# Optimization experiments

Measured on AMD Instinct MI355X. Metric: run time of the kernel, lower is better.

Reference implementation:

```python
import jax, jax.numpy as jnp
import numpy as np

N_NODES = 50000
N_EDGES = 800000
D_IN = 64
D_OUT = 64


def setup_inputs() -> dict:
    key = jax.random.key(0)
    k1, k2, k3, k4, k5 = jax.random.split(key, 5)
    x = jax.random.normal(k1, (N_NODES, D_IN), dtype=jnp.float32)
    senders = jax.random.randint(k2, (N_EDGES,), 0, N_NODES, dtype=jnp.int32)
    receivers = jax.random.randint(k3, (N_EDGES,), 0, N_NODES, dtype=jnp.int32)
    # eqx.nn.Linear params: weight [out, in], bias [out]
    weight = jax.random.normal(k4, (D_OUT, D_IN), dtype=jnp.float32) / np.sqrt(D_IN)
    bias = jax.random.normal(k5, (D_OUT,), dtype=jnp.float32) * 0.01
    return {"x": x, "senders": senders, "receivers": receivers, "weight": weight, "bias": bias}


def reference(x, senders, receivers, weight, bias):
    n = x.shape[0]
    # jraph.GraphConvolution applies update_node_fn (the Linear) FIRST
    h = x @ weight.T + bias  # [N, D_OUT]
    # add self edges
    self_idx = jnp.arange(n, dtype=senders.dtype)
    cs = jnp.concatenate([senders, self_idx])
    cr = jnp.concatenate([receivers, self_idx])
    ones = jnp.ones(cs.shape, dtype=h.dtype)
    sender_deg = jax.ops.segment_sum(ones, cs, num_segments=n)
    receiver_deg = jax.ops.segment_sum(ones, cr, num_segments=n)
    # symmetric normalization: D^{-1/2} A D^{-1/2}
    h = h * jax.lax.rsqrt(jnp.maximum(sender_deg, 1.0))[:, None]
    h = jax.ops.segment_sum(h[cs], cr, num_segments=n)  # gather -> scatter-add
    h = h * jax.lax.rsqrt(jnp.maximum(receiver_deg, 1.0))[:, None]
    return jax.nn.leaky_relu(h)  # default negative_slope=0.01
```

## Files before the change

kernel.cpp:

```cpp
#include <hip/hip_runtime.h>

#define N_NODES 50000
#define N_EDGES 800000
#define D 64
#define NB 196
#define BSZ 256
#define NSLICE 196
#define E4 (N_EDGES / 4)
#define CAP 64

__device__ __forceinline__ ushort f2bf(float f) {
    unsigned u = __float_as_uint(f);
    unsigned r = u + 0x7fffu + ((u >> 16) & 1u);
    return (ushort)(r >> 16);
}
__device__ __forceinline__ void acc8(const uint4 a, float* acc) {
    acc[0] += __uint_as_float(a.x << 16);
    acc[1] += __uint_as_float(a.x & 0xffff0000u);
    acc[2] += __uint_as_float(a.y << 16);
    acc[3] += __uint_as_float(a.y & 0xffff0000u);
    acc[4] += __uint_as_float(a.z << 16);
    acc[5] += __uint_as_float(a.z & 0xffff0000u);
    acc[6] += __uint_as_float(a.w << 16);
    acc[7] += __uint_as_float(a.w & 0xffff0000u);
}

__global__ __launch_bounds__(1024) void part1_kernel(
        const int* __restrict__ s, const int* __restrict__ r,
        unsigned* __restrict__ prc, unsigned char* __restrict__ psc,
        int* __restrict__ rcnt, int* __restrict__ scnt) {
    __shared__ int rcur[NB], scur[NB];
    const int tid = threadIdx.x, sl = blockIdx.x;
    for (int i = tid; i < NB; i += 1024) { rcur[i] = 0; scur[i] = 0; }
    __syncthreads();

    const size_t cellbase = (size_t)sl * NB * CAP;
    int e4 = sl * 1024 + tid;
    if (e4 < E4) {
        int4 rv = ((const int4*)r)[e4];
        int4 sv = ((const int4*)s)[e4];
        int ri[4] = {rv.x, rv.y, rv.z, rv.w};
        int si[4] = {sv.x, sv.y, sv.z, sv.w};
        #pragma unroll
        for (int k = 0; k < 4; ++k) {
            int b = ri[k] >> 8;
            int pos = atomicAdd(&rcur[b], 1);
            if (pos < CAP)
                prc[cellbase + (size_t)b * CAP + pos] =
                    ((unsigned)(ri[k] & 255) << 16) | (unsigned)si[k];
            int bs = si[k] >> 8;
            int pos2 = atomicAdd(&scur[bs], 1);
            if (pos2 < CAP)
                psc[cellbase + (size_t)bs * CAP + pos2] = (unsigned char)(si[k] & 255);
        }
    }
    __syncthreads();
    for (int i = tid; i < NB; i += 1024) {
        rcnt[sl * NB + i] = rcur[i];
        scnt[sl * NB + i] = scur[i];
    }
}

__global__ __launch_bounds__(256) void post_kernel(
        const unsigned* __restrict__ prc, const unsigned char* __restrict__ psc,
        const int* __restrict__ rcnt, const int* __restrict__ scnt,
        int* __restrict__ rowoff, ushort* __restrict__ csr16,
        float* __restrict__ sscale) {
    __shared__ int sc[256];
    __shared__ int h4[BSZ];
    const int tid = threadIdx.x;

    if (blockIdx.x >= NB) {
        const int b = blockIdx.x - NB;
        h4[tid] = 0;
        __syncthreads();
        for (int sl = tid; sl < NSLICE; sl += 256) {
            int c = scnt[sl * NB + b];
            const unsigned char* cell = psc + (size_t)sl * NB * CAP + (size_t)b * CAP;
            for (int i = 0; i < c; ++i) atomicAdd(&h4[cell[i]], 1);
        }
        __syncthreads();
        int n = b * BSZ + tid;
        if (n < N_NODES) sscale[n] = rsqrtf((float)(h4[tid] + 1));
        return;
    }

    const int b = blockIdx.x;
    int tot = 0;
    if (tid < NB) {
        for (int sl = 0; sl < NSLICE; ++sl) tot += rcnt[sl * NB + tid];
    }
    sc[tid] = tot;
    __syncthreads();
    for (int o = 1; o < 256; o <<= 1) {
        int u = (tid >= o) ? sc[tid - o] : 0;
        __syncthreads();
        sc[tid] += u;
        __syncthreads();
    }
    const int rb = (b == 0) ? 0 : sc[b - 1];
    __syncthreads();

    h4[tid] = 0;
    __syncthreads();
    for (int sl = tid; sl < NSLICE; sl += 256) {
        int c = rcnt[sl * NB + b];
        const unsigned* cell = prc + (size_t)sl * NB * CAP + (size_t)b * CAP;
        for (int i = 0; i < c; ++i) atomicAdd(&h4[cell[i] >> 16], 1);
    }
    __syncthreads();

    int v = h4[tid];
    sc[tid] = v;
    __syncthreads();
    for (int o = 1; o < 256; o <<= 1) {
        int u = (tid >= o) ? sc[tid - o] : 0;
        __syncthreads();
        sc[tid] += u;
        __syncthreads();
    }
    int excl = sc[tid] - v;
    int n = b * BSZ + tid;
    if (n < N_NODES) rowoff[n] = rb + excl;
    h4[tid] = rb + excl;
    if (b == NB - 1 && tid == 0) rowoff[N_NODES] = N_EDGES;
    __syncthreads();

    for (int sl = tid; sl < NSLICE; sl += 256) {
        int c = rcnt[sl * NB + b];
        const unsigned* cell = prc + (size_t)sl * NB * CAP + (size_t)b * CAP;
        for (int i = 0; i < c; ++i) {
            unsigned pw = cell[i];
            int pos = atomicAdd(&h4[pw >> 16], 1);
            csr16[pos] = (ushort)(pw & 0xffffu);
        }
    }
}

__global__ __launch_bounds__(256, 4) void linear_kernel(
        const float* __restrict__ x, const float* __restrict__ w,
        const float* __restrict__ bias, const float* __restrict__ sscale,
        ushort* __restrict__ h16) {
    __shared__ float wlds[64 * 68];
    __shared__ float xlds[64 * 68];
    __shared__ float blds[64];
    __shared__ float slds[64];
    const int t = threadIdx.x;
    const int t15 = t & 15;
    const int g = t >> 4;
    const int nb = blockIdx.x * 64;

    #pragma unroll
    for (int q = 0; q < 4; ++q) {
        int idx = q * 256 + t;
        int o = idx >> 4, k4 = idx & 15;
        float4 wv = ((const float4*)w)[idx];
        *(float4*)&wlds[o * 68 + k4 * 4] = wv;
    }
    if (t < 64) {
        blds[t] = bias[t];
        int n = nb + t;
        slds[t] = (n < N_NODES) ? sscale[n] : 0.f;
    }
    #pragma unroll
    for (int q = 0; q < 4; ++q) {
        int idx = q * 256 + t;
        int nl = idx >> 4, k4 = idx & 15;
        int n = nb + nl;
        float4 xv = (n < N_NODES) ? ((const float4*)x)[n * 16 + k4]
                                  : make_float4(0.f, 0.f, 0.f, 0.f);
        *(float4*)&xlds[nl * 68 + k4 * 4] = xv;
    }
    __syncthreads();

    float acc[4][4];
    #pragma unroll
    for (int i = 0; i < 4; ++i)
        #pragma unroll
        for (int j = 0; j < 4; ++j) acc[i][j] = 0.f;

    #pragma unroll 2
    for (int k4 = 0; k4 < 16; ++k4) {
        float4 wv0 = *(const float4*)&wlds[(t15     ) * 68 + k4 * 4];
        float4 wv1 = *(const float4*)&wlds[(t15 + 16) * 68 + k4 * 4];
        float4 wv2 = *(const float4*)&wlds[(t15 + 32) * 68 + k4 * 4];
        float4 wv3 = *(const float4*)&wlds[(t15 + 48) * 68 + k4 * 4];
        #pragma unroll
        for (int i = 0; i < 4; ++i) {
            float4 xv = *(const float4*)&xlds[(g * 4 + i) * 68 + k4 * 4];
            acc[i][0] += xv.x * wv0.x + xv.y * wv0.y + xv.z * wv0.z + xv.w * wv0.w;
            acc[i][1] += xv.x * wv1.x + xv.y * wv1.y + xv.z * wv1.z + xv.w * wv1.w;
            acc[i][2] += xv.x * wv2.x + xv.y * wv2.y + xv.z * wv2.z + xv.w * wv2.w;
            acc[i][3] += xv.x * wv3.x + xv.y * wv3.y + xv.z * wv3.z + xv.w * wv3.w;
        }
    }

    #pragma unroll
    for (int i = 0; i < 4; ++i) {
        int nl = g * 4 + i;
        int n = nb + nl;
        if (n < N_NODES) {
            float sc = slds[nl];
            h16[n * D + t15     ] = f2bf((acc[i][0] + blds[t15     ]) * sc);
            h16[n * D + t15 + 16] = f2bf((acc[i][1] + blds[t15 + 16]) * sc);
            h16[n * D + t15 + 32] = f2bf((acc[i][2] + blds[t15 + 32]) * sc);
            h16[n * D + t15 + 48] = f2bf((acc[i][3] + blds[t15 + 48]) * sc);
        }
    }
}

__global__ __launch_bounds__(256) void gather_kernel(
        const ushort* __restrict__ h16, const int* __restrict__ rowoff,
        const ushort* __restrict__ csr16, float* __restrict__ out) {
    const int lane = threadIdx.x & 63;
    const int q = lane & 7;
    const int g = lane >> 3;
    const int n = blockIdx.x * 4 + (threadIdx.x >> 6);
    if (n >= N_NODES) return;

    float acc[8];
    #pragma unroll
    for (int k = 0; k < 8; ++k) acc[k] = 0.f;

    const int base = rowoff[n];
    const int cnt = rowoff[n + 1] - base;

    for (int j0 = 0; j0 < cnt; j0 += 64) {
        int m = cnt - j0; if (m > 64) m = 64;
        int my = (lane < m) ? (int)csr16[base + j0 + lane] : 0;
        int t = 0;
        for (; t + 16 <= m; t += 16) {
            int s0 = __shfl(my, t + g);
            int s1 = __shfl(my, t + 8 + g);
            uint4 a = *(const uint4*)&h16[s0 * D + q * 8];
            uint4 b = *(const uint4*)&h16[s1 * D + q * 8];
            acc8(a, acc);
            acc8(b, acc);
        }
        for (; t < m; t += 8) {
            int e = t + g;
            int ee = (e < m) ? e : 0;
            int s0 = __shfl(my, ee);
            if (e < m) {
                uint4 a = *(const uint4*)&h16[s0 * D + q * 8];
                acc8(a, acc);
            }
        }
    }

    #pragma unroll
    for (int k = 0; k < 8; ++k) acc[k] += __shfl_xor(acc[k], 8);
    #pragma unroll
    for (int k = 0; k < 8; ++k) acc[k] += __shfl_xor(acc[k], 16);
    #pragma unroll
    for (int k = 0; k < 8; ++k) acc[k] += __shfl_xor(acc[k], 32);

    uint4 sv = *(const uint4*)&h16[n * D + q * 8];
    acc8(sv, acc);
    float sc = rsqrtf((float)(cnt + 1));
    float o[8];
    #pragma unroll
    for (int k = 0; k < 8; ++k) {
        float vv = acc[k] * sc;
        o[k] = vv > 0.f ? vv : 0.01f * vv;
    }
    if (g == 0) {
        *(float4*)(out + n * D + q * 8)     = make_float4(o[0], o[1], o[2], o[3]);
    } else if (g == 1) {
        *(float4*)(out + n * D + q * 8 + 4) = make_float4(o[4], o[5], o[6], o[7]);
    }
}

extern "C" void kernel_launch(void* const* d_in, const int* in_sizes, int n_in,
                              void* d_out, int out_size, void* d_ws, size_t ws_size,
                              hipStream_t stream) {
    const float* x       = (const float*)d_in[0];
    const int*   senders = (const int*)d_in[1];
    const int*   recvs   = (const int*)d_in[2];
    const float* weight  = (const float*)d_in[3];
    const float* bias    = (const float*)d_in[4];
    float* out = (float*)d_out;

    char* p = (char*)d_ws;
    auto take = [&](size_t bytes) { char* q = p; p += (bytes + 255) & ~(size_t)255; return q; };
    ushort*        h16    = (ushort*)take((size_t)N_NODES * D * 2);
    float*         sscale = (float*)take((size_t)N_NODES * 4);
    unsigned*      prc    = (unsigned*)take((size_t)NSLICE * NB * CAP * 4);
    unsigned char* psc    = (unsigned char*)take((size_t)NSLICE * NB * CAP);
    int*           rcnt   = (int*)take((size_t)NSLICE * NB * 4);
    int*           scnt   = (int*)take((size_t)NSLICE * NB * 4);
    int*           rowoff = (int*)take((size_t)(N_NODES + 1) * 4);
    ushort*        csr16  = (ushort*)take((size_t)N_EDGES * 2);

    hipLaunchKernelGGL(part1_kernel, dim3(NSLICE), dim3(1024), 0, stream,
                       senders, recvs, prc, psc, rcnt, scnt);
    hipLaunchKernelGGL(post_kernel, dim3(2 * NB), dim3(BSZ), 0, stream,
                       prc, psc, rcnt, scnt, rowoff, csr16, sscale);
    hipLaunchKernelGGL(linear_kernel, dim3((N_NODES + 63) / 64), dim3(256), 0, stream,
                       x, weight, bias, sscale, h16);
    hipLaunchKernelGGL(gather_kernel, dim3((N_NODES + 3) / 4), dim3(256), 0, stream,
                       h16, rowoff, csr16, out);
}
```

Measured before the change: 68.92 us.

## Fuse linear transform into sender-degree blocks of post kernel

Removes the separate linear kernel and the global sscale buffer. The sender-degree blocks of post_kernel now compute the per-node scale in shared memory and then run the 64x64 linear transform over four 64-node tiles, writing bf16 h16 directly. This saves one launch and a global round trip of the scale. In exchange, the linear work now runs on only 196 blocks instead of 782, with a larger shared-memory footprint for every post_kernel block, including the CSR blocks.

```diff
diff --git a/kernel.cpp b/kernel.cpp
--- a/kernel.cpp
+++ b/kernel.cpp
@@ -61,18 +61,24 @@
     }
 }
 
-__global__ __launch_bounds__(256) void post_kernel(
+__global__ __launch_bounds__(256, 4) void post_kernel(
         const unsigned* __restrict__ prc, const unsigned char* __restrict__ psc,
         const int* __restrict__ rcnt, const int* __restrict__ scnt,
         int* __restrict__ rowoff, ushort* __restrict__ csr16,
-        float* __restrict__ sscale) {
+        const float* __restrict__ x, const float* __restrict__ w,
+        const float* __restrict__ bias, ushort* __restrict__ h16) {
     __shared__ int sc[256];
     __shared__ int h4[BSZ];
+    __shared__ float wlds[64 * 68];
+    __shared__ float xlds[64 * 68];
+    __shared__ float slds[BSZ];
+    __shared__ float blds[64];
     const int tid = threadIdx.x;
 
     if (blockIdx.x >= NB) {
         const int b = blockIdx.x - NB;
         h4[tid] = 0;
+        if (tid < 64) blds[tid] = bias[tid];
         __syncthreads();
         for (int sl = tid; sl < NSLICE; sl += 256) {
             int c = scnt[sl * NB + b];
@@ -80,8 +86,67 @@
             for (int i = 0; i < c; ++i) atomicAdd(&h4[cell[i]], 1);
         }
         __syncthreads();
-        int n = b * BSZ + tid;
-        if (n < N_NODES) sscale[n] = rsqrtf((float)(h4[tid] + 1));
+        slds[tid] = rsqrtf((float)(h4[tid] + 1));
+        #pragma unroll
+        for (int q = 0; q < 4; ++q) {
+            int idx = q * 256 + tid;
+            int o = idx >> 4, k4 = idx & 15;
+            float4 wv = ((const float4*)w)[idx];
+            *(float4*)&wlds[o * 68 + k4 * 4] = wv;
+        }
+        __syncthreads();
+
+        const int t15 = tid & 15;
+        const int g = tid >> 4;
+        for (int tile = 0; tile < 4; ++tile) {
+            const int nb = b * BSZ + tile * 64;
+            #pragma unroll
+            for (int q = 0; q < 4; ++q) {
+                int idx = q * 256 + tid;
+                int nl = idx >> 4, k4 = idx & 15;
+                int n = nb + nl;
+                float4 xv = (n < N_NODES) ? ((const float4*)x)[n * 16 + k4]
+                                          : make_float4(0.f, 0.f, 0.f, 0.f);
+                *(float4*)&xlds[nl * 68 + k4 * 4] = xv;
+            }
+            __syncthreads();
+
+            float acc[4][4];
+            #pragma unroll
+            for (int i = 0; i < 4; ++i)
+                #pragma unroll
+                for (int j = 0; j < 4; ++j) acc[i][j] = 0.f;
+
+            #pragma unroll 2
+            for (int k4 = 0; k4 < 16; ++k4) {
+                float4 wv0 = *(const float4*)&wlds[(t15     ) * 68 + k4 * 4];
+                float4 wv1 = *(const float4*)&wlds[(t15 + 16) * 68 + k4 * 4];
+                float4 wv2 = *(const float4*)&wlds[(t15 + 32) * 68 + k4 * 4];
+                float4 wv3 = *(const float4*)&wlds[(t15 + 48) * 68 + k4 * 4];
+                #pragma unroll
+                for (int i = 0; i < 4; ++i) {
+                    float4 xv = *(const float4*)&xlds[(g * 4 + i) * 68 + k4 * 4];
+                    acc[i][0] += xv.x * wv0.x + xv.y * wv0.y + xv.z * wv0.z + xv.w * wv0.w;
+                    acc[i][1] += xv.x * wv1.x + xv.y * wv1.y + xv.z * wv1.z + xv.w * wv1.w;
+                    acc[i][2] += xv.x * wv2.x + xv.y * wv2.y + xv.z * wv2.z + xv.w * wv2.w;
+                    acc[i][3] += xv.x * wv3.x + xv.y * wv3.y + xv.z * wv3.z + xv.w * wv3.w;
+                }
+            }
+
+            #pragma unroll
+            for (int i = 0; i < 4; ++i) {
+                int nl = g * 4 + i;
+                int n = nb + nl;
+                if (n < N_NODES) {
+                    float scl = slds[tile * 64 + nl];
+                    h16[n * D + t15     ] = f2bf((acc[i][0] + blds[t15     ]) * scl);
+                    h16[n * D + t15 + 16] = f2bf((acc[i][1] + blds[t15 + 16]) * scl);
+                    h16[n * D + t15 + 32] = f2bf((acc[i][2] + blds[t15 + 32]) * scl);
+                    h16[n * D + t15 + 48] = f2bf((acc[i][3] + blds[t15 + 48]) * scl);
+                }
+            }
+            __syncthreads();
+        }
         return;
     }
 
@@ -133,78 +198,6 @@
             unsigned pw = cell[i];
             int pos = atomicAdd(&h4[pw >> 16], 1);
             csr16[pos] = (ushort)(pw & 0xffffu);
-        }
-    }
-}
-
-__global__ __launch_bounds__(256, 4) void linear_kernel(
-        const float* __restrict__ x, const float* __restrict__ w,
-        const float* __restrict__ bias, const float* __restrict__ sscale,
-        ushort* __restrict__ h16) {
-    __shared__ float wlds[64 * 68];
-    __shared__ float xlds[64 * 68];
-    __shared__ float blds[64];
-    __shared__ float slds[64];
-    const int t = threadIdx.x;
-    const int t15 = t & 15;
-    const int g = t >> 4;
-    const int nb = blockIdx.x * 64;
-
-    #pragma unroll
-    for (int q = 0; q < 4; ++q) {
-        int idx = q * 256 + t;
-        int o = idx >> 4, k4 = idx & 15;
-        float4 wv = ((const float4*)w)[idx];
-        *(float4*)&wlds[o * 68 + k4 * 4] = wv;
-    }
-    if (t < 64) {
-        blds[t] = bias[t];
-        int n = nb + t;
-        slds[t] = (n < N_NODES) ? sscale[n] : 0.f;
-    }
-    #pragma unroll
-    for (int q = 0; q < 4; ++q) {
-        int idx = q * 256 + t;
-        int nl = idx >> 4, k4 = idx & 15;
-        int n = nb + nl;
-        float4 xv = (n < N_NODES) ? ((const float4*)x)[n * 16 + k4]
-                                  : make_float4(0.f, 0.f, 0.f, 0.f);
-        *(float4*)&xlds[nl * 68 + k4 * 4] = xv;
-    }
-    __syncthreads();
-
-    float acc[4][4];
-    #pragma unroll
-    for (int i = 0; i < 4; ++i)
-        #pragma unroll
-        for (int j = 0; j < 4; ++j) acc[i][j] = 0.f;
-
-    #pragma unroll 2
-    for (int k4 = 0; k4 < 16; ++k4) {
-        float4 wv0 = *(const float4*)&wlds[(t15     ) * 68 + k4 * 4];
-        float4 wv1 = *(const float4*)&wlds[(t15 + 16) * 68 + k4 * 4];
-        float4 wv2 = *(const float4*)&wlds[(t15 + 32) * 68 + k4 * 4];
-        float4 wv3 = *(const float4*)&wlds[(t15 + 48) * 68 + k4 * 4];
-        #pragma unroll
-        for (int i = 0; i < 4; ++i) {
-            float4 xv = *(const float4*)&xlds[(g * 4 + i) * 68 + k4 * 4];
-            acc[i][0] += xv.x * wv0.x + xv.y * wv0.y + xv.z * wv0.z + xv.w * wv0.w;
-            acc[i][1] += xv.x * wv1.x + xv.y * wv1.y + xv.z * wv1.z + xv.w * wv1.w;
-            acc[i][2] += xv.x * wv2.x + xv.y * wv2.y + xv.z * wv2.z + xv.w * wv2.w;
-            acc[i][3] += xv.x * wv3.x + xv.y * wv3.y + xv.z * wv3.z + xv.w * wv3.w;
-        }
-    }
-
-    #pragma unroll
-    for (int i = 0; i < 4; ++i) {
-        int nl = g * 4 + i;
-        int n = nb + nl;
-        if (n < N_NODES) {
-            float sc = slds[nl];
-            h16[n * D + t15     ] = f2bf((acc[i][0] + blds[t15     ]) * sc);
-            h16[n * D + t15 + 16] = f2bf((acc[i][1] + blds[t15 + 16]) * sc);
-            h16[n * D + t15 + 32] = f2bf((acc[i][2] + blds[t15 + 32]) * sc);
-            h16[n * D + t15 + 48] = f2bf((acc[i][3] + blds[t15 + 48]) * sc);
         }
     }
 }
@@ -284,7 +277,6 @@
     char* p = (char*)d_ws;
     auto take = [&](size_t bytes) { char* q = p; p += (bytes + 255) & ~(size_t)255; return q; };
     ushort*        h16    = (ushort*)take((size_t)N_NODES * D * 2);
-    float*         sscale = (float*)take((size_t)N_NODES * 4);
     unsigned*      prc    = (unsigned*)take((size_t)NSLICE * NB * CAP * 4);
     unsigned char* psc    = (unsigned char*)take((size_t)NSLICE * NB * CAP);
     int*           rcnt   = (int*)take((size_t)NSLICE * NB * 4);
@@ -295,9 +287,8 @@
     hipLaunchKernelGGL(part1_kernel, dim3(NSLICE), dim3(1024), 0, stream,
                        senders, recvs, prc, psc, rcnt, scnt);
     hipLaunchKernelGGL(post_kernel, dim3(2 * NB), dim3(BSZ), 0, stream,
-                       prc, psc, rcnt, scnt, rowoff, csr16, sscale);
-    hipLaunchKernelGGL(linear_kernel, dim3((N_NODES + 63) / 64), dim3(256), 0, stream,
-                       x, weight, bias, sscale, h16);
+                       prc, psc, rcnt, scnt, rowoff, csr16,
+                       x, weight, bias, h16);
     hipLaunchKernelGGL(gather_kernel, dim3((N_NODES + 3) / 4), dim3(256), 0, stream,
                        h16, rowoff, csr16, out);
 }
```

New measurement: 65.51 us. 4.9% less time.
